# Performance work log

Hardware: AMD Instinct MI355X
Metric: run time of the kernel (lower is better)

Reference implementation:

```python
import jax, jax.numpy as jnp
import numpy as np

HEAD_SIZE = 64

def setup_inputs() -> dict:
    key = jax.random.key(0)
    ks = jax.random.split(key, 6)
    B, T, C = 4, 4096, 1024
    H = HEAD_SIZE
    return {
        "q": jax.random.normal(ks[0], (B, T, C), dtype=jnp.float32),
        "k": jax.random.normal(ks[1], (B, T, C), dtype=jnp.float32),
        "v": jax.random.normal(ks[2], (B, T, C), dtype=jnp.float32),
        "Wq": jax.random.normal(ks[3], (H, C), dtype=jnp.float32) * (C ** -0.5),
        "Wk": jax.random.normal(ks[4], (H, C), dtype=jnp.float32) * (C ** -0.5),
        "Wv": jax.random.normal(ks[5], (H, C), dtype=jnp.float32) * (C ** -0.5),
    }

def reference(q, k, v, Wq, Wk, Wv):
    # dropout p=0.0 -> identity (module applies F.dropout before each projection)
    T = q.shape[1]
    scale = HEAD_SIZE ** -0.5
    Q = jnp.einsum('btc,hc->bth', q, Wq)   # [B,T,H]
    K = jnp.einsum('btc,hc->bth', k, Wk)   # [B,T,H]
    V = jnp.einsum('btc,hc->bth', v, Wv)   # [B,T,H]
    scores = jnp.einsum('bth,bsh->bts', Q, K) * scale  # [B,T,T]
    # non-standard mask: tril with diagonal=1 (each query sees positions <= i+1)
    mask = jnp.tril(jnp.ones((T, T), dtype=bool), k=1)
    scores = jnp.where(mask, scores, -jnp.inf)
    # double scaling as in the original: softmax(scores * head_size**-0.5)
    weights = jax.nn.softmax(scores * scale, axis=-1)
    return jnp.einsum('bts,bsh->bth', weights, V)
```

## Files before the change

### kernel.cpp

```cpp
#include <hip/hip_runtime.h>
#include <hip/hip_bf16.h>

#define BB 4
#define TT 4096
#define CC 1024
#define HH 64

typedef _Float16 f16;
typedef __attribute__((ext_vector_type(8))) _Float16 f16x8;
typedef __attribute__((ext_vector_type(4))) _Float16 f16x4;
typedef __attribute__((ext_vector_type(4))) float f32x4;

#define MFMA32(a,b,c) __builtin_amdgcn_mfma_f32_16x16x32_f16((a),(b),(c),0,0,0)
#define MFMA16(a,b,c) __builtin_amdgcn_mfma_f32_16x16x16f16((a),(b),(c),0,0,0)

#define WF_ELEMS (3 * 32 * 4 * 64 * 8)
#define CHUNK_F16 1024
#define PB_F16 (256 * CHUNK_F16)

static __device__ __forceinline__ void gl_lds16(const void* g, void* l) {
  __builtin_amdgcn_global_load_lds(
      (const __attribute__((address_space(1))) unsigned int*)g,
      (__attribute__((address_space(3))) unsigned int*)l, 16, 0, 0);
}

static __device__ __forceinline__ f16x8 pack2(f32x4 a, f32x4 b) {
  f16x8 r;
  r[0]=(f16)a[0]; r[1]=(f16)a[1]; r[2]=(f16)a[2]; r[3]=(f16)a[3];
  r[4]=(f16)b[0]; r[5]=(f16)b[1]; r[6]=(f16)b[2]; r[7]=(f16)b[3];
  return r;
}

__global__ __launch_bounds__(64) void wrepack_kernel(
    const float* __restrict__ Wqg, const float* __restrict__ Wkg,
    const float* __restrict__ Wvg, f16* __restrict__ Wf)
{
  const int bx = blockIdx.x;
  const int nt = bx & 3;
  const int kc = (bx >> 2) & 31;
  const int p  = bx >> 7;
  const float* W = (p == 0) ? Wqg : (p == 1) ? Wkg : Wvg;
  const float sc = (p == 0) ? (1.4426950408889634f / 64.0f) : 1.0f;

  const int lane = threadIdx.x;
  const int l16 = lane & 15, quad = lane >> 4;
  const float* src = W + (size_t)(nt * 16 + l16) * CC + kc * 32 + quad * 8;
  f32x4 a = *(const f32x4*)src;
  f32x4 b = *(const f32x4*)(src + 4);
  f16x8 r;
  #pragma unroll
  for (int j = 0; j < 4; ++j) { r[j] = (f16)(a[j] * sc); r[j + 4] = (f16)(b[j] * sc); }
  *(f16x8*)(Wf + (size_t)bx * 512 + lane * 8) = r;
}

__global__ __launch_bounds__(256) void proj_kernel(
    const float* __restrict__ qg, const float* __restrict__ kg, const float* __restrict__ vg,
    const f16* __restrict__ Wf,
    f16* __restrict__ Qf, f16* __restrict__ Kf, f16* __restrict__ Vf)
{
  __shared__ float Xs[2][64][64];
  __shared__ f16   Ws[2][8][64][8];

  const float* X; f16* O; const int p = blockIdx.y;
  if (p == 0)      { X = qg; O = Qf; }
  else if (p == 1) { X = kg; O = Kf; }
  else             { X = vg; O = Vf; }

  const int tid  = threadIdx.x;
  const int w    = tid >> 6;
  const int lane = tid & 63;
  const int quad = lane >> 4;
  const int l16  = lane & 15;
  const int r0   = blockIdx.x * 64;

  const float* Xrow[4];
  #pragma unroll
  for (int s = 0; s < 4; ++s) {
    const int R  = w * 16 + s * 4 + (lane >> 4);
    const int lc = (lane & 15) ^ ((R & 7) << 1);
    Xrow[s] = X + (size_t)(r0 + R) * CC + lc * 4;
  }
  const f16* Wfp = Wf + (size_t)p * 128 * 512;
  const f16* Wsrc[2];
  #pragma unroll
  for (int jj = 0; jj < 2; ++jj)
    Wsrc[jj] = Wfp + (size_t)(2 * w + jj) * 512 + lane * 8;

  f32x4 acc[4];
  #pragma unroll
  for (int nt = 0; nt < 4; ++nt) acc[nt] = (f32x4){0.f, 0.f, 0.f, 0.f};

  #pragma unroll
  for (int s = 0; s < 4; ++s)
    gl_lds16(Xrow[s], &Xs[0][w * 16 + s * 4][0]);
  #pragma unroll
  for (int jj = 0; jj < 2; ++jj)
    gl_lds16(Wsrc[jj], &Ws[0][2 * w + jj][0][0]);

  const int sw = (l16 & 7) << 1;

  for (int it = 0; it < 16; ++it) {
    const int buf = it & 1;
    __syncthreads();
    if (it < 15) {
      #pragma unroll
      for (int s = 0; s < 4; ++s)
        gl_lds16(Xrow[s] + (it + 1) * 64, &Xs[buf ^ 1][w * 16 + s * 4][0]);
      #pragma unroll
      for (int jj = 0; jj < 2; ++jj)
        gl_lds16(Wsrc[jj] + (size_t)(it + 1) * 4096, &Ws[buf ^ 1][2 * w + jj][0][0]);
    }
    #pragma unroll
    for (int kk = 0; kk < 2; ++kk) {
      const int c0 = kk * 8 + quad * 2;
      f32x4 a0 = *(const f32x4*)&Xs[buf][w * 16 + l16][(c0 ^ sw) * 4];
      f32x4 a1 = *(const f32x4*)&Xs[buf][w * 16 + l16][((c0 + 1) ^ sw) * 4];
      f16x8 af = pack2(a0, a1);
      #pragma unroll
      for (int nt = 0; nt < 4; ++nt) {
        f16x8 bf = *(const f16x8*)&Ws[buf][kk * 4 + nt][lane][0];
        acc[nt] = MFMA32(af, bf, acc[nt]);
      }
    }
  }

  f16 (*Ls)[66] = (f16(*)[66])&Xs[0][w * 16][0];
  #pragma unroll
  for (int nt = 0; nt < 4; ++nt)
    #pragma unroll
    for (int r = 0; r < 4; ++r)
      Ls[quad * 4 + r][nt * 16 + l16] = (f16)acc[nt][r];
  const size_t chunk = (size_t)blockIdx.x * 4 + w;
  if (p < 2) {
    #pragma unroll
    for (int h = 0; h < 2; ++h) {
      f16x8 t = *(const f16x8*)&Ls[l16][h * 32 + quad * 8];
      *(f16x8*)(O + (chunk * 2 + h) * 512 + lane * 8) = t;
    }
  } else {
    #pragma unroll
    for (int np = 0; np < 2; ++np) {
      f16x8 t;
      #pragma unroll
      for (int j = 0; j < 8; ++j)
        t[j] = Ls[quad * 4 + (j & 3)][(2 * np + (j >> 2)) * 16 + l16];
      *(f16x8*)(O + (chunk * 2 + np) * 512 + lane * 8) = t;
    }
  }
}

__device__ __forceinline__ void attn_tile(
    int b, int j, int a, int e, int wave, int quad, int l16, int lane, int sp,
    const f16* __restrict__ Qf, const f16* __restrict__ Kf, const f16* __restrict__ Vf,
    f16 (*Ks)[8][64][8], f16 (*Vs)[8][64][8],
    float* __restrict__ Opart, float* __restrict__ lpart)
{
  const int m0 = j * 64 + wave * 16;

  const f16* Kfb = Kf + (size_t)b * PB_F16;
  const f16* Vfb = Vf + (size_t)b * PB_F16;
  const f16* Qfb = Qf + (size_t)b * PB_F16;

  f16x8 qa0 = *(const f16x8*)(Qfb + ((size_t)(m0 >> 4) * 2 + 0) * 512 + lane * 8);
  f16x8 qa1 = *(const f16x8*)(Qfb + ((size_t)(m0 >> 4) * 2 + 1) * 512 + lane * 8);

  f32x4 o[4];
  float lsum = 0.f;
  #pragma unroll
  for (int nt = 0; nt < 4; ++nt) o[nt] = (f32x4){0.f, 0.f, 0.f, 0.f};

  __syncthreads();

  if (a < e) {
    #pragma unroll
    for (int jj = 0; jj < 2; ++jj) {
      const int idx = 2 * wave + jj;
      gl_lds16(Kfb + (size_t)a * 4096 + idx * 512 + lane * 8, &Ks[0][idx][0][0]);
      gl_lds16(Vfb + (size_t)a * 4096 + idx * 512 + lane * 8, &Vs[0][idx][0][0]);
    }
  }

  for (int st = a; st < e; ++st) {
    const int buf = (st - a) & 1;
    __syncthreads();
    if (st + 1 < e) {
      #pragma unroll
      for (int jj = 0; jj < 2; ++jj) {
        const int idx = 2 * wave + jj;
        gl_lds16(Kfb + (size_t)(st + 1) * 4096 + idx * 512 + lane * 8, &Ks[buf ^ 1][idx][0][0]);
        gl_lds16(Vfb + (size_t)(st + 1) * 4096 + idx * 512 + lane * 8, &Vs[buf ^ 1][idx][0][0]);
      }
    }
    const int s0 = st * 64;

    f32x4 sc[4];
    #pragma unroll
    for (int ct = 0; ct < 4; ++ct) {
      f16x8 k0 = *(const f16x8*)&Ks[buf][ct * 2][lane][0];
      f16x8 k1 = *(const f16x8*)&Ks[buf][ct * 2 + 1][lane][0];
      f32x4 z = (f32x4){0.f, 0.f, 0.f, 0.f};
      z = MFMA32(k0, qa0, z);
      sc[ct] = MFMA32(k1, qa1, z);
    }

    const bool domask = (s0 + 63) > (m0 + 1);
    f16x4 pa[4];
    #pragma unroll
    for (int ct = 0; ct < 4; ++ct) {
      #pragma unroll
      for (int r = 0; r < 4; ++r) {
        float x = sc[ct][r];
        if (domask) {
          const int key = s0 + ct * 16 + quad * 4 + r;
          if (key > m0 + l16 + 1) x = -__builtin_inff();
        }
        const float pv = __builtin_amdgcn_exp2f(x);
        lsum += pv;
        pa[ct][r] = (f16)pv;
      }
    }

    #pragma unroll
    for (int ct = 0; ct < 4; ++ct) {
      #pragma unroll
      for (int np = 0; np < 2; ++np) {
        f16x8 vv = *(const f16x8*)&Vs[buf][ct * 2 + np][lane][0];
        f16x4 blo = __builtin_shufflevector(vv, vv, 0, 1, 2, 3);
        f16x4 bhi = __builtin_shufflevector(vv, vv, 4, 5, 6, 7);
        o[2 * np]     = MFMA16(pa[ct], blo, o[2 * np]);
        o[2 * np + 1] = MFMA16(pa[ct], bhi, o[2 * np + 1]);
      }
    }
  }

  lsum += __shfl_xor(lsum, 16, 64);
  lsum += __shfl_xor(lsum, 32, 64);
  const size_t rbase = (size_t)(sp * BB + b) * TT;
  if (quad == 0) lpart[rbase + m0 + l16] = lsum;
  #pragma unroll
  for (int nt = 0; nt < 4; ++nt)
    #pragma unroll
    for (int r = 0; r < 4; ++r)
      Opart[(rbase + m0 + quad * 4 + r) * HH + nt * 16 + l16] = o[nt][r];
}

__global__ __launch_bounds__(256) void attn_kernel(
    const f16* __restrict__ Qf, const f16* __restrict__ Kf, const f16* __restrict__ Vf,
    float* __restrict__ Opart, float* __restrict__ lpart, int S)
{
  __shared__ f16 Ks[2][8][64][8];
  __shared__ f16 Vs[2][8][64][8];

  const int pr = blockIdx.x;
  const int sp = blockIdx.y;
  const int b  = blockIdx.z;
  const int tid  = threadIdx.x;
  const int wave = tid >> 6;
  const int lane = tid & 63;
  const int quad = lane >> 4;
  const int l16  = lane & 15;

  const int j1 = pr, j2 = 63 - pr;
  const int n1 = min(j1 + 2, 64), n2 = min(j2 + 2, 64);
  const int tot = n1 + n2;
  const int lo = tot * sp / S, hi = tot * (sp + 1) / S;
  const int a1 = min(lo, n1), e1 = min(hi, n1);
  const int a2 = max(lo - n1, 0), e2 = max(hi - n1, 0);

  attn_tile(b, j1, a1, e1, wave, quad, l16, lane, sp, Qf, Kf, Vf, Ks, Vs, Opart, lpart);
  attn_tile(b, j2, a2, e2, wave, quad, l16, lane, sp, Qf, Kf, Vf, Ks, Vs, Opart, lpart);
}

__global__ __launch_bounds__(256) void combine_kernel(
    const float* __restrict__ Opart, const float* __restrict__ lpart,
    float* __restrict__ out, int S)
{
  const int idx = blockIdx.x * 256 + threadIdx.x;
  const int row = idx >> 4;
  const int c   = (idx & 15) * 4;
  float l = 0.f;
  f32x4 s = (f32x4){0.f, 0.f, 0.f, 0.f};
  for (int p = 0; p < S; ++p) {
    l += lpart[(size_t)p * BB * TT + row];
    s += *(const f32x4*)&Opart[((size_t)p * BB * TT + row) * HH + c];
  }
  const float inv = 1.0f / l;
  *(f32x4*)&out[(size_t)row * HH + c] = s * inv;
}

extern "C" void kernel_launch(void* const* d_in, const int* in_sizes, int n_in,
                              void* d_out, int out_size, void* d_ws, size_t ws_size,
                              hipStream_t stream)
{
  const float* q  = (const float*)d_in[0];
  const float* k  = (const float*)d_in[1];
  const float* v  = (const float*)d_in[2];
  const float* Wq = (const float*)d_in[3];
  const float* Wk = (const float*)d_in[4];
  const float* Wv = (const float*)d_in[5];
  float* out = (float*)d_out;

  const size_t n = (size_t)BB * TT * HH;
  const size_t need8 = (WF_ELEMS + 3 * n) * sizeof(f16)
                     + 8 * n * sizeof(float) + 8 * (size_t)BB * TT * sizeof(float);
  const int S = (ws_size >= need8) ? 8 : 4;

  f16* Wf = (f16*)d_ws;
  f16* Qf = Wf + WF_ELEMS;
  f16* Kf = Qf + n;
  f16* Vf = Kf + n;
  float* Opart = (float*)(Vf + n);
  float* lpart = Opart + (size_t)S * n;

  wrepack_kernel<<<dim3(384), 64, 0, stream>>>(Wq, Wk, Wv, Wf);
  proj_kernel<<<dim3(256, 3), 256, 0, stream>>>(q, k, v, Wf, Qf, Kf, Vf);
  attn_kernel<<<dim3(32, S, BB), 256, 0, stream>>>(Qf, Kf, Vf, Opart, lpart, S);
  combine_kernel<<<dim3(1024), 256, 0, stream>>>(Opart, lpart, out, S);
}
```

Measured before the change: 235.5 us.

## Share K/V tiles between paired query tiles and widen projection blocks

The attention kernel now walks the key range once per block and applies each loaded K/V tile to both paired query tiles (j and 63-j). It drops the separate per-tile passes that reloaded the same K/V data, and uses per-wave bounds to skip the fully masked extra key tile for waves that do not need it. The projection kernel moves to 512 threads and 128 rows per block, so each staged weight chunk is reused across twice as many rows. This raises register use (both accumulator sets plus cached K/V fragments) and changes how work is balanced across the split dimension.

```diff
diff --git a/kernel.cpp b/kernel.cpp
--- a/kernel.cpp
+++ b/kernel.cpp
@@ -53,12 +53,12 @@
   *(f16x8*)(Wf + (size_t)bx * 512 + lane * 8) = r;
 }
 
-__global__ __launch_bounds__(256) void proj_kernel(
+__global__ __launch_bounds__(512) void proj_kernel(
     const float* __restrict__ qg, const float* __restrict__ kg, const float* __restrict__ vg,
     const f16* __restrict__ Wf,
     f16* __restrict__ Qf, f16* __restrict__ Kf, f16* __restrict__ Vf)
 {
-  __shared__ float Xs[2][64][64];
+  __shared__ float Xs[2][128][64];
   __shared__ f16   Ws[2][8][64][8];
 
   const float* X; f16* O; const int p = blockIdx.y;
@@ -71,7 +71,7 @@
   const int lane = tid & 63;
   const int quad = lane >> 4;
   const int l16  = lane & 15;
-  const int r0   = blockIdx.x * 64;
+  const int r0   = blockIdx.x * 128;
 
   const float* Xrow[4];
   #pragma unroll
@@ -81,10 +81,7 @@
     Xrow[s] = X + (size_t)(r0 + R) * CC + lc * 4;
   }
   const f16* Wfp = Wf + (size_t)p * 128 * 512;
-  const f16* Wsrc[2];
-  #pragma unroll
-  for (int jj = 0; jj < 2; ++jj)
-    Wsrc[jj] = Wfp + (size_t)(2 * w + jj) * 512 + lane * 8;
+  const f16* Wsrc = Wfp + (size_t)w * 512 + lane * 8;
 
   f32x4 acc[4];
   #pragma unroll
@@ -93,9 +90,7 @@
   #pragma unroll
   for (int s = 0; s < 4; ++s)
     gl_lds16(Xrow[s], &Xs[0][w * 16 + s * 4][0]);
-  #pragma unroll
-  for (int jj = 0; jj < 2; ++jj)
-    gl_lds16(Wsrc[jj], &Ws[0][2 * w + jj][0][0]);
+  gl_lds16(Wsrc, &Ws[0][w][0][0]);
 
   const int sw = (l16 & 7) << 1;
 
@@ -106,9 +101,7 @@
       #pragma unroll
       for (int s = 0; s < 4; ++s)
         gl_lds16(Xrow[s] + (it + 1) * 64, &Xs[buf ^ 1][w * 16 + s * 4][0]);
-      #pragma unroll
-      for (int jj = 0; jj < 2; ++jj)
-        gl_lds16(Wsrc[jj] + (size_t)(it + 1) * 4096, &Ws[buf ^ 1][2 * w + jj][0][0]);
+      gl_lds16(Wsrc + (size_t)(it + 1) * 4096, &Ws[buf ^ 1][w][0][0]);
     }
     #pragma unroll
     for (int kk = 0; kk < 2; ++kk) {
@@ -130,7 +123,7 @@
     #pragma unroll
     for (int r = 0; r < 4; ++r)
       Ls[quad * 4 + r][nt * 16 + l16] = (f16)acc[nt][r];
-  const size_t chunk = (size_t)blockIdx.x * 4 + w;
+  const size_t chunk = (size_t)blockIdx.x * 8 + w;
   if (p < 2) {
     #pragma unroll
     for (int h = 0; h < 2; ++h) {
@@ -147,101 +140,6 @@
       *(f16x8*)(O + (chunk * 2 + np) * 512 + lane * 8) = t;
     }
   }
-}
-
-__device__ __forceinline__ void attn_tile(
-    int b, int j, int a, int e, int wave, int quad, int l16, int lane, int sp,
-    const f16* __restrict__ Qf, const f16* __restrict__ Kf, const f16* __restrict__ Vf,
-    f16 (*Ks)[8][64][8], f16 (*Vs)[8][64][8],
-    float* __restrict__ Opart, float* __restrict__ lpart)
-{
-  const int m0 = j * 64 + wave * 16;
-
-  const f16* Kfb = Kf + (size_t)b * PB_F16;
-  const f16* Vfb = Vf + (size_t)b * PB_F16;
-  const f16* Qfb = Qf + (size_t)b * PB_F16;
-
-  f16x8 qa0 = *(const f16x8*)(Qfb + ((size_t)(m0 >> 4) * 2 + 0) * 512 + lane * 8);
-  f16x8 qa1 = *(const f16x8*)(Qfb + ((size_t)(m0 >> 4) * 2 + 1) * 512 + lane * 8);
-
-  f32x4 o[4];
-  float lsum = 0.f;
-  #pragma unroll
-  for (int nt = 0; nt < 4; ++nt) o[nt] = (f32x4){0.f, 0.f, 0.f, 0.f};
-
-  __syncthreads();
-
-  if (a < e) {
-    #pragma unroll
-    for (int jj = 0; jj < 2; ++jj) {
-      const int idx = 2 * wave + jj;
-      gl_lds16(Kfb + (size_t)a * 4096 + idx * 512 + lane * 8, &Ks[0][idx][0][0]);
-      gl_lds16(Vfb + (size_t)a * 4096 + idx * 512 + lane * 8, &Vs[0][idx][0][0]);
-    }
-  }
-
-  for (int st = a; st < e; ++st) {
-    const int buf = (st - a) & 1;
-    __syncthreads();
-    if (st + 1 < e) {
-      #pragma unroll
-      for (int jj = 0; jj < 2; ++jj) {
-        const int idx = 2 * wave + jj;
-        gl_lds16(Kfb + (size_t)(st + 1) * 4096 + idx * 512 + lane * 8, &Ks[buf ^ 1][idx][0][0]);
-        gl_lds16(Vfb + (size_t)(st + 1) * 4096 + idx * 512 + lane * 8, &Vs[buf ^ 1][idx][0][0]);
-      }
-    }
-    const int s0 = st * 64;
-
-    f32x4 sc[4];
-    #pragma unroll
-    for (int ct = 0; ct < 4; ++ct) {
-      f16x8 k0 = *(const f16x8*)&Ks[buf][ct * 2][lane][0];
-      f16x8 k1 = *(const f16x8*)&Ks[buf][ct * 2 + 1][lane][0];
-      f32x4 z = (f32x4){0.f, 0.f, 0.f, 0.f};
-      z = MFMA32(k0, qa0, z);
-      sc[ct] = MFMA32(k1, qa1, z);
-    }
-
-    const bool domask = (s0 + 63) > (m0 + 1);
-    f16x4 pa[4];
-    #pragma unroll
-    for (int ct = 0; ct < 4; ++ct) {
-      #pragma unroll
-      for (int r = 0; r < 4; ++r) {
-        float x = sc[ct][r];
-        if (domask) {
-          const int key = s0 + ct * 16 + quad * 4 + r;
-          if (key > m0 + l16 + 1) x = -__builtin_inff();
-        }
-        const float pv = __builtin_amdgcn_exp2f(x);
-        lsum += pv;
-        pa[ct][r] = (f16)pv;
-      }
-    }
-
-    #pragma unroll
-    for (int ct = 0; ct < 4; ++ct) {
-      #pragma unroll
-      for (int np = 0; np < 2; ++np) {
-        f16x8 vv = *(const f16x8*)&Vs[buf][ct * 2 + np][lane][0];
-        f16x4 blo = __builtin_shufflevector(vv, vv, 0, 1, 2, 3);
-        f16x4 bhi = __builtin_shufflevector(vv, vv, 4, 5, 6, 7);
-        o[2 * np]     = MFMA16(pa[ct], blo, o[2 * np]);
-        o[2 * np + 1] = MFMA16(pa[ct], bhi, o[2 * np + 1]);
-      }
-    }
-  }
-
-  lsum += __shfl_xor(lsum, 16, 64);
-  lsum += __shfl_xor(lsum, 32, 64);
-  const size_t rbase = (size_t)(sp * BB + b) * TT;
-  if (quad == 0) lpart[rbase + m0 + l16] = lsum;
-  #pragma unroll
-  for (int nt = 0; nt < 4; ++nt)
-    #pragma unroll
-    for (int r = 0; r < 4; ++r)
-      Opart[(rbase + m0 + quad * 4 + r) * HH + nt * 16 + l16] = o[nt][r];
 }
 
 __global__ __launch_bounds__(256) void attn_kernel(
@@ -261,14 +159,147 @@
   const int l16  = lane & 15;
 
   const int j1 = pr, j2 = 63 - pr;
-  const int n1 = min(j1 + 2, 64), n2 = min(j2 + 2, 64);
-  const int tot = n1 + n2;
-  const int lo = tot * sp / S, hi = tot * (sp + 1) / S;
-  const int a1 = min(lo, n1), e1 = min(hi, n1);
-  const int a2 = max(lo - n1, 0), e2 = max(hi - n1, 0);
-
-  attn_tile(b, j1, a1, e1, wave, quad, l16, lane, sp, Qf, Kf, Vf, Ks, Vs, Opart, lpart);
-  attn_tile(b, j2, a2, e2, wave, quad, l16, lane, sp, Qf, Kf, Vf, Ks, Vs, Opart, lpart);
+  const int n2 = min(j2 + 2, 64);
+  const int lo = n2 * sp / S, hi = n2 * (sp + 1) / S;
+
+  const int m1 = j1 * 64 + wave * 16;
+  const int m2 = j2 * 64 + wave * 16;
+  const int e1 = min(hi, j1 + 1 + (wave == 3 ? 1 : 0));
+  const int e2 = min(hi, j2 + 1 + (wave == 3 ? 1 : 0));
+
+  const f16* Qfb = Qf + (size_t)b * PB_F16;
+  const f16* Kfb = Kf + (size_t)b * PB_F16;
+  const f16* Vfb = Vf + (size_t)b * PB_F16;
+
+  f16x8 qa10 = *(const f16x8*)(Qfb + ((size_t)(m1 >> 4) * 2 + 0) * 512 + lane * 8);
+  f16x8 qa11 = *(const f16x8*)(Qfb + ((size_t)(m1 >> 4) * 2 + 1) * 512 + lane * 8);
+  f16x8 qa20 = *(const f16x8*)(Qfb + ((size_t)(m2 >> 4) * 2 + 0) * 512 + lane * 8);
+  f16x8 qa21 = *(const f16x8*)(Qfb + ((size_t)(m2 >> 4) * 2 + 1) * 512 + lane * 8);
+
+  f32x4 o1[4], o2[4];
+  float ls1 = 0.f, ls2 = 0.f;
+  #pragma unroll
+  for (int nt = 0; nt < 4; ++nt) {
+    o1[nt] = (f32x4){0.f, 0.f, 0.f, 0.f};
+    o2[nt] = (f32x4){0.f, 0.f, 0.f, 0.f};
+  }
+
+  if (lo < hi) {
+    const int idx = 2 * wave;
+    #pragma unroll
+    for (int jj = 0; jj < 2; ++jj) {
+      gl_lds16(Kfb + (size_t)lo * 4096 + (idx + jj) * 512 + lane * 8, &Ks[0][idx + jj][0][0]);
+      gl_lds16(Vfb + (size_t)lo * 4096 + (idx + jj) * 512 + lane * 8, &Vs[0][idx + jj][0][0]);
+    }
+  }
+
+  for (int st = lo; st < hi; ++st) {
+    const int buf = (st - lo) & 1;
+    __syncthreads();
+    if (st + 1 < hi) {
+      const int idx = 2 * wave;
+      #pragma unroll
+      for (int jj = 0; jj < 2; ++jj) {
+        gl_lds16(Kfb + (size_t)(st + 1) * 4096 + (idx + jj) * 512 + lane * 8, &Ks[buf ^ 1][idx + jj][0][0]);
+        gl_lds16(Vfb + (size_t)(st + 1) * 4096 + (idx + jj) * 512 + lane * 8, &Vs[buf ^ 1][idx + jj][0][0]);
+      }
+    }
+    const int s0 = st * 64;
+
+    f16x8 kf[8]; f16x8 vf[8];
+    #pragma unroll
+    for (int i = 0; i < 8; ++i) {
+      kf[i] = *(const f16x8*)&Ks[buf][i][lane][0];
+      vf[i] = *(const f16x8*)&Vs[buf][i][lane][0];
+    }
+
+    if (st < e1) {
+      f32x4 sc[4];
+      #pragma unroll
+      for (int ct = 0; ct < 4; ++ct) {
+        f32x4 z = (f32x4){0.f, 0.f, 0.f, 0.f};
+        z = MFMA32(kf[2 * ct], qa10, z);
+        sc[ct] = MFMA32(kf[2 * ct + 1], qa11, z);
+      }
+      const bool domask = (s0 + 63) > (m1 + 1);
+      f16x4 pa[4];
+      #pragma unroll
+      for (int ct = 0; ct < 4; ++ct)
+        #pragma unroll
+        for (int r = 0; r < 4; ++r) {
+          float x = sc[ct][r];
+          if (domask) {
+            const int key = s0 + ct * 16 + quad * 4 + r;
+            if (key > m1 + l16 + 1) x = -__builtin_inff();
+          }
+          const float pv = __builtin_amdgcn_exp2f(x);
+          ls1 += pv;
+          pa[ct][r] = (f16)pv;
+        }
+      #pragma unroll
+      for (int ct = 0; ct < 4; ++ct)
+        #pragma unroll
+        for (int np = 0; np < 2; ++np) {
+          f16x8 vv = vf[2 * ct + np];
+          f16x4 blo = __builtin_shufflevector(vv, vv, 0, 1, 2, 3);
+          f16x4 bhi = __builtin_shufflevector(vv, vv, 4, 5, 6, 7);
+          o1[2 * np]     = MFMA16(pa[ct], blo, o1[2 * np]);
+          o1[2 * np + 1] = MFMA16(pa[ct], bhi, o1[2 * np + 1]);
+        }
+    }
+
+    if (st < e2) {
+      f32x4 sc[4];
+      #pragma unroll
+      for (int ct = 0; ct < 4; ++ct) {
+        f32x4 z = (f32x4){0.f, 0.f, 0.f, 0.f};
+        z = MFMA32(kf[2 * ct], qa20, z);
+        sc[ct] = MFMA32(kf[2 * ct + 1], qa21, z);
+      }
+      const bool domask = (s0 + 63) > (m2 + 1);
+      f16x4 pa[4];
+      #pragma unroll
+      for (int ct = 0; ct < 4; ++ct)
+        #pragma unroll
+        for (int r = 0; r < 4; ++r) {
+          float x = sc[ct][r];
+          if (domask) {
+            const int key = s0 + ct * 16 + quad * 4 + r;
+            if (key > m2 + l16 + 1) x = -__builtin_inff();
+          }
+          const float pv = __builtin_amdgcn_exp2f(x);
+          ls2 += pv;
+          pa[ct][r] = (f16)pv;
+        }
+      #pragma unroll
+      for (int ct = 0; ct < 4; ++ct)
+        #pragma unroll
+        for (int np = 0; np < 2; ++np) {
+          f16x8 vv = vf[2 * ct + np];
+          f16x4 blo = __builtin_shufflevector(vv, vv, 0, 1, 2, 3);
+          f16x4 bhi = __builtin_shufflevector(vv, vv, 4, 5, 6, 7);
+          o2[2 * np]     = MFMA16(pa[ct], blo, o2[2 * np]);
+          o2[2 * np + 1] = MFMA16(pa[ct], bhi, o2[2 * np + 1]);
+        }
+    }
+  }
+
+  ls1 += __shfl_xor(ls1, 16, 64);
+  ls1 += __shfl_xor(ls1, 32, 64);
+  ls2 += __shfl_xor(ls2, 16, 64);
+  ls2 += __shfl_xor(ls2, 32, 64);
+  const size_t rbase = (size_t)(sp * BB + b) * TT;
+  if (quad == 0) {
+    lpart[rbase + m1 + l16] = ls1;
+    lpart[rbase + m2 + l16] = ls2;
+  }
+  #pragma unroll
+  for (int nt = 0; nt < 4; ++nt)
+    #pragma unroll
+    for (int r = 0; r < 4; ++r) {
+      Opart[(rbase + m1 + quad * 4 + r) * HH + nt * 16 + l16] = o1[nt][r];
+      Opart[(rbase + m2 + quad * 4 + r) * HH + nt * 16 + l16] = o2[nt][r];
+    }
 }
 
 __global__ __launch_bounds__(256) void combine_kernel(
@@ -313,7 +344,7 @@
   float* lpart = Opart + (size_t)S * n;
 
   wrepack_kernel<<<dim3(384), 64, 0, stream>>>(Wq, Wk, Wv, Wf);
-  proj_kernel<<<dim3(256, 3), 256, 0, stream>>>(q, k, v, Wf, Qf, Kf, Vf);
+  proj_kernel<<<dim3(128, 3), 512, 0, stream>>>(q, k, v, Wf, Qf, Kf, Vf);
   attn_kernel<<<dim3(32, S, BB), 256, 0, stream>>>(Qf, Kf, Vf, Opart, lpart, S);
   combine_kernel<<<dim3(1024), 256, 0, stream>>>(Opart, lpart, out, S);
 }
```

Result: slower. 246.6 us (+4.7%).
